# Kernel tuning notes

Hardware: AMD Instinct MI355X
Metric: run time of the kernel (lower is better)

The kernel has to match this reference:

```python
import jax, jax.numpy as jnp
import numpy as np

B, T, U = 64, 1000, 200
D, H, V = 1024, 512, 100  # decoder_dim, hidden_size, vocab_size; blank id = V
NEG = -1e30


def setup_inputs() -> dict:
    key = jax.random.key(0)
    ks = jax.random.split(key, 6)
    decoder_outputs = jax.random.normal(ks[0], (B, T, D), dtype=jnp.float32)
    target_phones = jax.random.randint(ks[1], (B, U), 0, V)
    decoder_lengths = T // 2 + jax.random.randint(ks[2], (B,), 0, T // 2 + 1)
    target_lengths = U // 2 + jax.random.randint(ks[3], (B,), 0, U // 2 + 1)
    W1 = jax.random.normal(ks[4], (H, D), dtype=jnp.float32) * (1.0 / np.sqrt(D))
    b1 = jnp.zeros((H,), jnp.float32)
    W2 = jax.random.normal(ks[5], (V + 1, H), dtype=jnp.float32) * (1.0 / np.sqrt(H))
    b2 = jnp.zeros((V + 1,), jnp.float32)
    return dict(decoder_outputs=decoder_outputs, target_phones=target_phones,
                decoder_lengths=decoder_lengths, target_lengths=target_lengths,
                W1=W1, b1=b1, W2=W2, b2=b2)


def _lse3(a, b, c):
    m = jnp.maximum(jnp.maximum(a, b), c)
    return m + jnp.log(jnp.exp(a - m) + jnp.exp(b - m) + jnp.exp(c - m))


def _ctc_loss(log_probs, targets, in_len, tgt_len, blank):
    # log_probs: [B, T, C]; targets: [B, U]; standard CTC alpha recursion in log space.
    Bb, Tt, _ = log_probs.shape
    Uu = targets.shape[1]
    S = 2 * Uu + 1  # extended label sequence: blank, y1, blank, y2, ...
    ext = jnp.full((Bb, S), blank, dtype=targets.dtype).at[:, 1::2].set(targets)
    lp = jnp.take_along_axis(log_probs, ext[:, None, :], axis=2)  # [B, T, S]
    same = jnp.concatenate([jnp.ones((Bb, 2), bool), ext[:, 2:] == ext[:, :-2]], axis=1)
    skip_ok = (ext != blank) & (~same)  # allowed s-2 transition

    a0 = jnp.full((Bb, S), NEG, jnp.float32).at[:, 0].set(lp[:, 0, 0]).at[:, 1].set(lp[:, 0, 1])
    lp_t = jnp.swapaxes(lp, 0, 1)  # [T, B, S]

    def step(alpha, xs):
        t, lpt = xs
        a1 = jnp.concatenate([jnp.full((Bb, 1), NEG, jnp.float32), alpha[:, :-1]], axis=1)
        a2 = jnp.concatenate([jnp.full((Bb, 2), NEG, jnp.float32), alpha[:, :-2]], axis=1)
        a2 = jnp.where(skip_ok, a2, NEG)
        new = _lse3(alpha, a1, a2) + lpt
        alpha = jnp.where((t < in_len)[:, None], new, alpha)  # freeze past each seq's end
        return alpha, None

    alpha, _ = jax.lax.scan(step, a0, (jnp.arange(1, Tt), lp_t[1:]))
    Sb = 2 * tgt_len + 1
    l1 = jnp.take_along_axis(alpha, (Sb - 1)[:, None], axis=1)[:, 0]
    l2 = jnp.take_along_axis(alpha, (Sb - 2)[:, None], axis=1)[:, 0]
    return -jnp.logaddexp(l1, l2)  # [B] per-sequence negative log likelihood


def reference(decoder_outputs, target_phones, decoder_lengths, target_lengths, W1, b1, W2, b2):
    # proj: Linear + ReLU (+ Dropout, identity in eval)
    h = jax.nn.relu(jnp.einsum('btd,hd->bth', decoder_outputs, W1) + b1)
    logits = jnp.einsum('bth,ch->btc', h, W2) + b2  # [B, T, V+1]
    log_probs = jax.nn.log_softmax(logits, axis=2)
    loss = _ctc_loss(log_probs, target_phones, decoder_lengths, target_lengths, blank=V)
    return jnp.mean(loss / decoder_lengths.astype(jnp.float32))
```

## Files before the change

### kernel.cpp

```cpp
#include <hip/hip_runtime.h>
#include <cstdint>
#include <cstddef>

#define NEGF (-1e30f)
#define LOG2E 1.4426950408889634f
#define LN2 0.6931471805599453f

typedef __attribute__((ext_vector_type(8))) short short8;
typedef __attribute__((ext_vector_type(4))) float f32x4;

__device__ __forceinline__ unsigned short f2bf(float f) {
  unsigned int u = __float_as_uint(f);
  u += 0x7fffu + ((u >> 16) & 1u);
  return (unsigned short)(u >> 16);
}

__device__ __forceinline__ void gload_lds16(const void* g, void* l) {
  __builtin_amdgcn_global_load_lds(
      (const __attribute__((address_space(1))) void*)g,
      (__attribute__((address_space(3))) void*)l, 16, 0, 0);
}

__device__ __forceinline__ float fexp2(float x) { return __builtin_amdgcn_exp2f(x); }
__device__ __forceinline__ float flog2(float x) { return __builtin_amdgcn_logf(x); }

__device__ __forceinline__ float wave_shr1(float x, float fill) {
  int r = __builtin_amdgcn_update_dpp(__float_as_int(fill), __float_as_int(x),
                                      0x138, 0xF, 0xF, false);
  return __int_as_float(r);
}

__device__ __forceinline__ float lse3_2(float a, float b, float c) {
  float m  = fmaxf(fmaxf(a, b), c);
  float md = __builtin_amdgcn_fmed3f(a, b, c);
  float mn = fminf(fminf(a, b), c);
  return m + flog2(fexp2(md - m) + fexp2(mn - m) + 1.0f);
}

__global__ void k_cvt(const float* __restrict__ src, unsigned short* __restrict__ dst, long n) {
  long i = ((long)blockIdx.x * blockDim.x + threadIdx.x) * 4;
  long stride = (long)gridDim.x * blockDim.x * 4;
  for (; i < n; i += stride) {
    float4 v = *(const float4*)(src + i);
    ushort4 o;
    o.x = f2bf(v.x); o.y = f2bf(v.y); o.z = f2bf(v.z); o.w = f2bf(v.w);
    *(ushort4*)(dst + i) = o;
  }
}

__global__ void k_cvt_w2(const float* __restrict__ w2, unsigned short* __restrict__ dst) {
  int i = (blockIdx.x * blockDim.x + threadIdx.x) * 4;
  if (i >= 128 * 512) return;
  int c = i >> 9;
  float4 v = make_float4(0.f, 0.f, 0.f, 0.f);
  if (c < 101) v = *(const float4*)(w2 + i);
  ushort4 o;
  o.x = f2bf(v.x); o.y = f2bf(v.y); o.z = f2bf(v.z); o.w = f2bf(v.w);
  *(ushort4*)(dst + i) = o;
}

__global__ __launch_bounds__(512, 1) void k_gemm1f(
    const float* __restrict__ X,
    const unsigned short* __restrict__ B,
    const float* __restrict__ b1,
    const int* __restrict__ dlen,
    unsigned short* __restrict__ H) {
  __shared__ __align__(16) char ldsA[128 * 144];
  __shared__ __align__(16) char ldsB[65536];
  const int K = 1024;
  int r0 = blockIdx.x * 128;
  {
    int b0 = r0 / 1000;
    int rl = r0 - b0 * 1000;
    if (rl <= 872 && rl >= dlen[b0]) return;
  }
  int tid = threadIdx.x;
  int lane = tid & 63, wid = tid >> 6;
  int wr = (wid & 1) * 64;
  int wc = (wid >> 1) * 128;

  f32x4 acc[4][8];
#pragma unroll
  for (int i = 0; i < 4; ++i)
#pragma unroll
    for (int j = 0; j < 8; ++j) acc[i][j] = (f32x4){0.f, 0.f, 0.f, 0.f};

  int arow = tid >> 2;
  int akoff = (tid & 3) * 16;

  for (int kt = 0; kt < 16; ++kt) {
    int k0 = kt * 64;
    __syncthreads();
    {
      const float* ap = X + (size_t)(r0 + arow) * K + (k0 + akoff);
      float4 av0 = *(const float4*)(ap + 0);
      float4 av1 = *(const float4*)(ap + 4);
      float4 av2 = *(const float4*)(ap + 8);
      float4 av3 = *(const float4*)(ap + 12);
      short8 as0, as1;
      as0[0] = (short)f2bf(av0.x); as0[1] = (short)f2bf(av0.y);
      as0[2] = (short)f2bf(av0.z); as0[3] = (short)f2bf(av0.w);
      as0[4] = (short)f2bf(av1.x); as0[5] = (short)f2bf(av1.y);
      as0[6] = (short)f2bf(av1.z); as0[7] = (short)f2bf(av1.w);
      as1[0] = (short)f2bf(av2.x); as1[1] = (short)f2bf(av2.y);
      as1[2] = (short)f2bf(av2.z); as1[3] = (short)f2bf(av2.w);
      as1[4] = (short)f2bf(av3.x); as1[5] = (short)f2bf(av3.y);
      as1[6] = (short)f2bf(av3.z); as1[7] = (short)f2bf(av3.w);
      int ab = arow * 144 + akoff * 2;
      *(short8*)(ldsA + ab) = as0;
      *(short8*)(ldsA + ab + 16) = as1;
    }
#pragma unroll
    for (int r = 0; r < 8; ++r) {
      int c = r * 512 + tid;
      int trow = c >> 3;
      int sch = (c & 7) ^ (trow & 7);
      gload_lds16(B + (size_t)trow * K + (k0 + sch * 8), ldsB + c * 16);
    }
    asm volatile("s_waitcnt vmcnt(0)" ::: "memory");
    __syncthreads();
#pragma unroll
    for (int kk = 0; kk < 2; ++kk) {
      int kb2 = (kk * 32 + ((lane >> 4) << 3)) * 2;
      short8 af[4], bfr[8];
#pragma unroll
      for (int i = 0; i < 4; ++i) {
        int ar = wr + i * 16 + (lane & 15);
        af[i] = *(const short8*)(ldsA + (ar * 144 + kb2));
      }
#pragma unroll
      for (int j = 0; j < 8; ++j) {
        int br = wc + j * 16 + (lane & 15);
        bfr[j] = *(const short8*)(ldsB + ((br * 128 + kb2) ^ ((br & 7) << 4)));
      }
#pragma unroll
      for (int i = 0; i < 4; ++i)
#pragma unroll
        for (int j = 0; j < 8; ++j)
          acc[i][j] = __builtin_amdgcn_mfma_f32_16x16x32_bf16(af[i], bfr[j], acc[i][j], 0, 0, 0);
    }
  }
  int cl = lane & 15, r4 = (lane >> 4) << 2;
#pragma unroll
  for (int i = 0; i < 4; ++i) {
    int row = r0 + wr + i * 16 + r4;
#pragma unroll
    for (int j = 0; j < 8; ++j) {
      int col = wc + j * 16 + cl;
      float bb = b1[col];
#pragma unroll
      for (int q = 0; q < 4; ++q) {
        float v = acc[i][j][q] + bb;
        v = v > 0.f ? v : 0.f;
        H[(size_t)(row + q) * 512 + col] = f2bf(v);
      }
    }
  }
}

__global__ __launch_bounds__(256) void k_gemm2(
    const unsigned short* __restrict__ Hm,
    const unsigned short* __restrict__ W2,
    const float* __restrict__ b2,
    const int* __restrict__ dlen,
    float* __restrict__ LPT) {
  __shared__ __align__(16) char lds[32768];
  const int K = 512;
  int row0 = blockIdx.x * 128;
  {
    int b0 = row0 / 1000;
    int rl = row0 - b0 * 1000;
    if (rl <= 872 && rl >= dlen[b0]) return;
  }
  int tid = threadIdx.x, lane = tid & 63, wid = tid >> 6;
  f32x4 acc[2][8];
#pragma unroll
  for (int i = 0; i < 2; ++i)
#pragma unroll
    for (int j = 0; j < 8; ++j) acc[i][j] = (f32x4){0.f, 0.f, 0.f, 0.f};

  for (int kt = 0; kt < 8; ++kt) {
    int k0 = kt * 64;
    __syncthreads();
#pragma unroll
    for (int r = 0; r < 4; ++r) {
      int c = r * 256 + tid;
      int trow = c >> 3;
      int sch = (c & 7) ^ (trow & 7);
      gload_lds16(Hm + (size_t)(row0 + trow) * K + (k0 + sch * 8), lds + c * 16);
      gload_lds16(W2 + (size_t)trow * K + (k0 + sch * 8), lds + 16384 + c * 16);
    }
    asm volatile("s_waitcnt vmcnt(0)" ::: "memory");
    __syncthreads();
#pragma unroll
    for (int kk = 0; kk < 2; ++kk) {
      int kb2 = (kk * 32 + ((lane >> 4) << 3)) * 2;
      short8 af[2], bfr[8];
#pragma unroll
      for (int i = 0; i < 2; ++i) {
        int ar = wid * 32 + i * 16 + (lane & 15);
        af[i] = *(const short8*)(lds + ((ar * 128 + kb2) ^ ((ar & 7) << 4)));
      }
#pragma unroll
      for (int j = 0; j < 8; ++j) {
        int br = j * 16 + (lane & 15);
        bfr[j] = *(const short8*)(lds + 16384 + ((br * 128 + kb2) ^ ((br & 7) << 4)));
      }
#pragma unroll
      for (int i = 0; i < 2; ++i)
#pragma unroll
        for (int j = 0; j < 8; ++j)
          acc[i][j] = __builtin_amdgcn_mfma_f32_16x16x32_bf16(af[i], bfr[j], acc[i][j], 0, 0, 0);
    }
  }
  int cl = lane & 15, r4 = (lane >> 4) << 2;
#pragma unroll
  for (int i = 0; i < 2; ++i) {
    float outv[4][8];
#pragma unroll
    for (int q = 0; q < 4; ++q) {
      float v[8];
      float mx = NEGF;
#pragma unroll
      for (int j = 0; j < 8; ++j) {
        int col = j * 16 + cl;
        float t = acc[i][j][q];
        if (col < 101) {
          t += b2[col];
          mx = fmaxf(mx, t);
        }
        v[j] = t;
      }
#pragma unroll
      for (int m = 1; m < 16; m <<= 1) mx = fmaxf(mx, __shfl_xor(mx, m));
      float s = 0.f;
#pragma unroll
      for (int j = 0; j < 8; ++j) {
        int col = j * 16 + cl;
        if (col < 101) s += __expf(v[j] - mx);
      }
#pragma unroll
      for (int m = 1; m < 16; m <<= 1) s += __shfl_xor(s, m);
      float lse = mx + __logf(s);
#pragma unroll
      for (int j = 0; j < 8; ++j) outv[q][j] = (v[j] - lse) * LOG2E;
    }
    int row = row0 + wid * 32 + i * 16 + r4;
    int bb = row / 1000;
    int t = row - bb * 1000;
    float* outp = LPT + (size_t)bb * 101000 + t;
#pragma unroll
    for (int j = 0; j < 8; ++j) {
      int col = j * 16 + cl;
      if (col < 101) {
        float4 o = make_float4(outv[0][j], outv[1][j], outv[2][j], outv[3][j]);
        *(float4*)(outp + col * 1000) = o;
      }
    }
  }
}

__global__ __launch_bounds__(256, 1) void k_ctc(
    const float* __restrict__ LPT,
    const int* __restrict__ tgt_all,
    const int* __restrict__ dlen,
    const int* __restrict__ tlen,
    float* __restrict__ lossout) {
  int b = blockIdx.x;
  int tid = threadIdx.x;
  int lane = tid & 63, wid = tid >> 6;
  const float* lpt = LPT + (size_t)b * 101000;
  int Tb = dlen[b];
  int Ub = tlen[b];
  const int* tg = tgt_all + b * 200;

  int h = (wid == 0) ? 0 : 16;
  int S0 = 101 * wid - h;
  int g0 = S0 + 2 * lane;

  int cls[2], sk[2];
#pragma unroll
  for (int j = 0; j < 2; ++j) {
    int s = g0 + j;
    int c = 100, skp = 0;
    if (s >= 0 && s < 401 && (s & 1)) {
      int u = (s - 1) >> 1;
      c = tg[u];
      if (s >= 3) skp = (tg[u] != tg[u - 1]) ? 1 : 0;
    }
    cls[j] = c; sk[j] = skp;
  }

  const float* pa = lpt + cls[0] * 1000;
  const float* pb = lpt + cls[1] * 1000;

  float al0 = (g0 == 0) ? pa[0] : NEGF;
  float al1 = (g0 == 0) ? pb[0] : NEGF;

  int slot_base = (wid == 0) ? 85 : 101;
  int e0 = 2 * lane - slot_base;

  __shared__ float bnd[2][3][16];
  __shared__ float sal[408];

  float4 a_lo0 = *(const float4*)(pa + 0),  a_lo1 = *(const float4*)(pa + 4);
  float4 a_hi0 = *(const float4*)(pa + 8),  a_hi1 = *(const float4*)(pa + 12);
  float4 b_lo0 = *(const float4*)(pb + 0),  b_lo1 = *(const float4*)(pb + 4);
  float4 b_hi0 = *(const float4*)(pb + 8),  b_hi1 = *(const float4*)(pb + 12);

#define STEP(tt, PA, PB)                                                  \
  do {                                                                    \
    if ((tt) < Tb) {                                                      \
      float u1 = wave_shr1(al1, NEGF);           \
      float u0 = wave_shr1(al0, NEGF);           \
      float na0 = lse3_2(al0, u1, sk[0] ? u0 : NEGF) + (PA);              \
      float na1 = lse3_2(al1, al0, sk[1] ? u1 : NEGF) + (PB);             \
      al0 = na0; al1 = na1;                                               \
    }                                                                     \
  } while (0)

  for (int t = 1; t < Tb; t += 8) {
    int buf = (t >> 3) & 1;
    if (wid < 3) {
      if (e0 >= 0 && e0 < 16) bnd[buf][wid][e0] = al0;
      int e1 = e0 + 1;
      if (e1 >= 0 && e1 < 16) bnd[buf][wid][e1] = al1;
    }
    __syncthreads();
    if (wid > 0 && lane < 8) {
      al0 = bnd[buf][wid - 1][2 * lane];
      al1 = bnd[buf][wid - 1][2 * lane + 1];
    }
    STEP(t,     a_lo0.y, b_lo0.y);
    STEP(t + 1, a_lo0.z, b_lo0.z);
    STEP(t + 2, a_lo0.w, b_lo0.w);
    STEP(t + 3, a_lo1.x, b_lo1.x);
    STEP(t + 4, a_lo1.y, b_lo1.y);
    STEP(t + 5, a_lo1.z, b_lo1.z);
    STEP(t + 6, a_lo1.w, b_lo1.w);
    STEP(t + 7, a_hi0.x, b_hi0.x);
    a_lo0 = a_hi0; a_lo1 = a_hi1;
    b_lo0 = b_hi0; b_lo1 = b_hi1;
    int tn = t + 15;
    a_hi0 = *(const float4*)(pa + tn); a_hi1 = *(const float4*)(pa + tn + 4);
    b_hi0 = *(const float4*)(pb + tn); b_hi1 = *(const float4*)(pb + tn + 4);
  }

  {
    int slot0 = 2 * lane;
    if (slot0 >= h && slot0 < h + 101 && g0 >= 0 && g0 <= 400) sal[g0] = al0;
    int slot1 = slot0 + 1, g1 = g0 + 1;
    if (slot1 >= h && slot1 < h + 101 && g1 <= 400) sal[g1] = al1;
  }
  __syncthreads();
  if (tid == 0) {
    float l1 = sal[2 * Ub];
    float l2 = sal[2 * Ub - 1];
    float m = fmaxf(l1, l2);
    float l2sum = m + flog2(fexp2(l1 - m) + fexp2(l2 - m));
    lossout[b] = (-LN2 * l2sum) / (float)Tb;
  }
#undef STEP
}

__global__ void k_reduce(const float* __restrict__ lossv, float* __restrict__ out) {
  float v = lossv[threadIdx.x];
#pragma unroll
  for (int m = 1; m < 64; m <<= 1) v += __shfl_xor(v, m);
  if (threadIdx.x == 0) out[0] = v * (1.0f / 64.0f);
}

extern "C" void kernel_launch(void* const* d_in, const int* in_sizes, int n_in,
                              void* d_out, int out_size, void* d_ws, size_t ws_size,
                              hipStream_t stream) {
  const float* X  = (const float*)d_in[0];
  const int* tgt  = (const int*)d_in[1];
  const int* dlen = (const int*)d_in[2];
  const int* tlen = (const int*)d_in[3];
  const float* W1 = (const float*)d_in[4];
  const float* b1 = (const float*)d_in[5];
  const float* W2 = (const float*)d_in[6];
  const float* b2 = (const float*)d_in[7];

  char* ws = (char*)d_ws;
  float* LPT           = (float*)(ws + 33554432);
  unsigned short* W1bf = (unsigned short*)(ws + 131072000);
  unsigned short* W2bf = (unsigned short*)(ws + 132120576);
  unsigned short* Hbf  = (unsigned short*)(ws + 132251648);
  float* lossv         = (float*)(ws + 197787648);

  k_cvt<<<512, 256, 0, stream>>>(W1, W1bf, 524288L);
  k_cvt_w2<<<64, 256, 0, stream>>>(W2, W2bf);
  k_gemm1f<<<500, 512, 0, stream>>>(X, W1bf, b1, dlen, Hbf);
  k_gemm2<<<500, 256, 0, stream>>>(Hbf, W2bf, b2, dlen, LPT);
  k_ctc<<<64, 256, 0, stream>>>(LPT, tgt, dlen, tlen, lossv);
  k_reduce<<<1, 64, 0, stream>>>(lossv, (float*)d_out);
}
```

Before: 246.2 us.

## Run CTC recursion in probability space with mantissa/exponent pairs

```diff
diff --git a/kernel.cpp b/kernel.cpp
--- a/kernel.cpp
+++ b/kernel.cpp
@@ -3,8 +3,8 @@
 #include <cstddef>
 
 #define NEGF (-1e30f)
-#define LOG2E 1.4426950408889634f
 #define LN2 0.6931471805599453f
+#define EMIN (-100000000)
 
 typedef __attribute__((ext_vector_type(8))) short short8;
 typedef __attribute__((ext_vector_type(4))) float f32x4;
@@ -29,12 +29,8 @@
                                       0x138, 0xF, 0xF, false);
   return __int_as_float(r);
 }
-
-__device__ __forceinline__ float lse3_2(float a, float b, float c) {
-  float m  = fmaxf(fmaxf(a, b), c);
-  float md = __builtin_amdgcn_fmed3f(a, b, c);
-  float mn = fminf(fminf(a, b), c);
-  return m + flog2(fexp2(md - m) + fexp2(mn - m) + 1.0f);
+__device__ __forceinline__ int wave_shr1_i(int x, int fill) {
+  return __builtin_amdgcn_update_dpp(fill, x, 0x138, 0xF, 0xF, false);
 }
 
 __global__ void k_cvt(const float* __restrict__ src, unsigned short* __restrict__ dst, long n) {
@@ -163,7 +159,7 @@
     const unsigned short* __restrict__ W2,
     const float* __restrict__ b2,
     const int* __restrict__ dlen,
-    float* __restrict__ LPT) {
+    float* __restrict__ PT) {
   __shared__ __align__(16) char lds[32768];
   const int K = 512;
   int row0 = blockIdx.x * 128;
@@ -243,12 +239,12 @@
       for (int m = 1; m < 16; m <<= 1) s += __shfl_xor(s, m);
       float lse = mx + __logf(s);
 #pragma unroll
-      for (int j = 0; j < 8; ++j) outv[q][j] = (v[j] - lse) * LOG2E;
+      for (int j = 0; j < 8; ++j) outv[q][j] = __expf(v[j] - lse);
     }
     int row = row0 + wid * 32 + i * 16 + r4;
     int bb = row / 1000;
     int t = row - bb * 1000;
-    float* outp = LPT + (size_t)bb * 101000 + t;
+    float* outp = PT + (size_t)bb * 101000 + t;
 #pragma unroll
     for (int j = 0; j < 8; ++j) {
       int col = j * 16 + cl;
@@ -261,7 +257,7 @@
 }
 
 __global__ __launch_bounds__(256, 1) void k_ctc(
-    const float* __restrict__ LPT,
+    const float* __restrict__ PT,
     const int* __restrict__ tgt_all,
     const int* __restrict__ dlen,
     const int* __restrict__ tlen,
@@ -269,7 +265,7 @@
   int b = blockIdx.x;
   int tid = threadIdx.x;
   int lane = tid & 63, wid = tid >> 6;
-  const float* lpt = LPT + (size_t)b * 101000;
+  const float* pt = PT + (size_t)b * 101000;
   int Tb = dlen[b];
   int Ub = tlen[b];
   const int* tg = tgt_all + b * 200;
@@ -291,17 +287,23 @@
     cls[j] = c; sk[j] = skp;
   }
 
-  const float* pa = lpt + cls[0] * 1000;
-  const float* pb = lpt + cls[1] * 1000;
-
-  float al0 = (g0 == 0) ? pa[0] : NEGF;
-  float al1 = (g0 == 0) ? pb[0] : NEGF;
+  const float* pa = pt + cls[0] * 1000;
+  const float* pb = pt + cls[1] * 1000;
+
+  float m0 = 0.f, m1 = 0.f;
+  int E0 = EMIN, E1 = EMIN;
+  if (g0 == 0) {
+    m0 = frexpf(pa[0], &E0);
+    m1 = frexpf(pb[0], &E1);
+  }
 
   int slot_base = (wid == 0) ? 85 : 101;
-  int e0 = 2 * lane - slot_base;
-
-  __shared__ float bnd[2][3][16];
-  __shared__ float sal[408];
+  int e0x = 2 * lane - slot_base;
+
+  __shared__ float bnd_m[2][3][16];
+  __shared__ int   bnd_e[2][3][16];
+  __shared__ float sal_m[408];
+  __shared__ int   sal_e[408];
 
   float4 a_lo0 = *(const float4*)(pa + 0),  a_lo1 = *(const float4*)(pa + 4);
   float4 a_hi0 = *(const float4*)(pa + 8),  a_hi1 = *(const float4*)(pa + 12);
@@ -311,25 +313,36 @@
 #define STEP(tt, PA, PB)                                                  \
   do {                                                                    \
     if ((tt) < Tb) {                                                      \
-      float u1 = wave_shr1(al1, NEGF);           \
-      float u0 = wave_shr1(al0, NEGF);           \
-      float na0 = lse3_2(al0, u1, sk[0] ? u0 : NEGF) + (PA);              \
-      float na1 = lse3_2(al1, al0, sk[1] ? u1 : NEGF) + (PB);             \
-      al0 = na0; al1 = na1;                                               \
+      float m1p = wave_shr1(m1, 0.f);                                     \
+      float m0p = wave_shr1(m0, 0.f);                                     \
+      int   E1p = wave_shr1_i(E1, EMIN);                                  \
+      int   E0p = wave_shr1_i(E0, EMIN);                                  \
+      float A2 = sk[0] ? m0p : 0.f;  int B2 = sk[0] ? E0p : EMIN;         \
+      int em0 = max(E0, max(E1p, B2));                                    \
+      float t0 = ldexpf(m0, E0 - em0) + ldexpf(m1p, E1p - em0)            \
+               + ldexpf(A2, B2 - em0);                                    \
+      t0 *= (PA);                                                         \
+      float C2 = sk[1] ? m1p : 0.f;  int D2 = sk[1] ? E1p : EMIN;         \
+      int em1 = max(E1, max(E0, D2));                                     \
+      float t1 = ldexpf(m1, E1 - em1) + ldexpf(m0, E0 - em1)              \
+               + ldexpf(C2, D2 - em1);                                    \
+      t1 *= (PB);                                                         \
+      int x0; m0 = frexpf(t0, &x0); E0 = em0 + x0;                        \
+      int x1; m1 = frexpf(t1, &x1); E1 = em1 + x1;                        \
     }                                                                     \
   } while (0)
 
   for (int t = 1; t < Tb; t += 8) {
     int buf = (t >> 3) & 1;
     if (wid < 3) {
-      if (e0 >= 0 && e0 < 16) bnd[buf][wid][e0] = al0;
-      int e1 = e0 + 1;
-      if (e1 >= 0 && e1 < 16) bnd[buf][wid][e1] = al1;
+      if (e0x >= 0 && e0x < 16) { bnd_m[buf][wid][e0x] = m0; bnd_e[buf][wid][e0x] = E0; }
+      int e1x = e0x + 1;
+      if (e1x >= 0 && e1x < 16) { bnd_m[buf][wid][e1x] = m1; bnd_e[buf][wid][e1x] = E1; }
     }
     __syncthreads();
     if (wid > 0 && lane < 8) {
-      al0 = bnd[buf][wid - 1][2 * lane];
-      al1 = bnd[buf][wid - 1][2 * lane + 1];
+      m0 = bnd_m[buf][wid - 1][2 * lane];     E0 = bnd_e[buf][wid - 1][2 * lane];
+      m1 = bnd_m[buf][wid - 1][2 * lane + 1]; E1 = bnd_e[buf][wid - 1][2 * lane + 1];
     }
     STEP(t,     a_lo0.y, b_lo0.y);
     STEP(t + 1, a_lo0.z, b_lo0.z);
@@ -348,17 +361,21 @@
 
   {
     int slot0 = 2 * lane;
-    if (slot0 >= h && slot0 < h + 101 && g0 >= 0 && g0 <= 400) sal[g0] = al0;
+    if (slot0 >= h && slot0 < h + 101 && g0 >= 0 && g0 <= 400) {
+      sal_m[g0] = m0; sal_e[g0] = E0;
+    }
     int slot1 = slot0 + 1, g1 = g0 + 1;
-    if (slot1 >= h && slot1 < h + 101 && g1 <= 400) sal[g1] = al1;
+    if (slot1 >= h && slot1 < h + 101 && g1 <= 400) {
+      sal_m[g1] = m1; sal_e[g1] = E1;
+    }
   }
   __syncthreads();
   if (tid == 0) {
-    float l1 = sal[2 * Ub];
-    float l2 = sal[2 * Ub - 1];
-    float m = fmaxf(l1, l2);
-    float l2sum = m + flog2(fexp2(l1 - m) + fexp2(l2 - m));
-    lossout[b] = (-LN2 * l2sum) / (float)Tb;
+    float ma = sal_m[2 * Ub], mb = sal_m[2 * Ub - 1];
+    int ea = sal_e[2 * Ub], eb = sal_e[2 * Ub - 1];
+    int em = max(ea, eb);
+    float val = ldexpf(ma, ea - em) + ldexpf(mb, eb - em);
+    lossout[b] = (-LN2 * ((float)em + flog2(val))) / (float)Tb;
   }
 #undef STEP
 }
@@ -383,7 +400,7 @@
   const float* b2 = (const float*)d_in[7];
 
   char* ws = (char*)d_ws;
-  float* LPT           = (float*)(ws + 33554432);
+  float* PT            = (float*)(ws + 33554432);
   unsigned short* W1bf = (unsigned short*)(ws + 131072000);
   unsigned short* W2bf = (unsigned short*)(ws + 132120576);
   unsigned short* Hbf  = (unsigned short*)(ws + 132251648);
@@ -392,7 +409,7 @@
   k_cvt<<<512, 256, 0, stream>>>(W1, W1bf, 524288L);
   k_cvt_w2<<<64, 256, 0, stream>>>(W2, W2bf);
   k_gemm1f<<<500, 512, 0, stream>>>(X, W1bf, b1, dlen, Hbf);
-  k_gemm2<<<500, 256, 0, stream>>>(Hbf, W2bf, b2, dlen, LPT);
-  k_ctc<<<64, 256, 0, stream>>>(LPT, tgt, dlen, tlen, lossv);
+  k_gemm2<<<500, 256, 0, stream>>>(Hbf, W2bf, b2, dlen, PT);
+  k_ctc<<<64, 256, 0, stream>>>(PT, tgt, dlen, tlen, lossv);
   k_reduce<<<1, 64, 0, stream>>>(lossv, (float*)d_out);
 }
```

Result: no change. 248.9 us (+1.1%).

## Fuse hidden projection GEMM and output GEMM with log-softmax into one kernel

Applied to the files above, without the earlier changes.

```diff
diff --git a/kernel.cpp b/kernel.cpp
--- a/kernel.cpp
+++ b/kernel.cpp
@@ -59,14 +59,17 @@
   *(ushort4*)(dst + i) = o;
 }
 
-__global__ __launch_bounds__(512, 1) void k_gemm1f(
+__global__ __launch_bounds__(512, 1) void k_fused(
     const float* __restrict__ X,
-    const unsigned short* __restrict__ B,
+    const unsigned short* __restrict__ W1b,
     const float* __restrict__ b1,
+    const unsigned short* __restrict__ W2b,
+    const float* __restrict__ b2,
     const int* __restrict__ dlen,
-    unsigned short* __restrict__ H) {
-  __shared__ __align__(16) char ldsA[128 * 144];
-  __shared__ __align__(16) char ldsB[65536];
+    float* __restrict__ LPT) {
+  __shared__ __align__(16) char lds[131072];
+  char* ldsA = lds;
+  char* ldsB = lds + 18432;
   const int K = 1024;
   int r0 = blockIdx.x * 128;
   {
@@ -115,7 +118,7 @@
       int c = r * 512 + tid;
       int trow = c >> 3;
       int sch = (c & 7) ^ (trow & 7);
-      gload_lds16(B + (size_t)trow * K + (k0 + sch * 8), ldsB + c * 16);
+      gload_lds16(W1b + (size_t)trow * K + (k0 + sch * 8), ldsB + c * 16);
     }
     asm volatile("s_waitcnt vmcnt(0)" ::: "memory");
     __syncthreads();
@@ -140,82 +143,48 @@
           acc[i][j] = __builtin_amdgcn_mfma_f32_16x16x32_bf16(af[i], bfr[j], acc[i][j], 0, 0, 0);
     }
   }
-  int cl = lane & 15, r4 = (lane >> 4) << 2;
-#pragma unroll
-  for (int i = 0; i < 4; ++i) {
-    int row = r0 + wr + i * 16 + r4;
+
+  __syncthreads();
+  {
+    int cl = lane & 15, r4 = (lane >> 4) << 2;
 #pragma unroll
     for (int j = 0; j < 8; ++j) {
-      int col = wc + j * 16 + cl;
-      float bb = b1[col];
-#pragma unroll
-      for (int q = 0; q < 4; ++q) {
-        float v = acc[i][j][q] + bb;
-        v = v > 0.f ? v : 0.f;
-        H[(size_t)(row + q) * 512 + col] = f2bf(v);
-      }
-    }
-  }
-}
-
-__global__ __launch_bounds__(256) void k_gemm2(
-    const unsigned short* __restrict__ Hm,
-    const unsigned short* __restrict__ W2,
-    const float* __restrict__ b2,
-    const int* __restrict__ dlen,
-    float* __restrict__ LPT) {
-  __shared__ __align__(16) char lds[32768];
-  const int K = 512;
-  int row0 = blockIdx.x * 128;
+      int hcol = wc + j * 16 + cl;
+      float bb = b1[hcol];
+      int cb = (hcol & 7) * 2;
+      int ch = hcol >> 3;
+#pragma unroll
+      for (int i = 0; i < 4; ++i) {
+#pragma unroll
+        for (int q = 0; q < 4; ++q) {
+          int hrow = wr + i * 16 + r4 + q;
+          float v = acc[i][j][q] + bb;
+          v = v > 0.f ? v : 0.f;
+          *(unsigned short*)(lds + hrow * 1024 + ((ch ^ (hrow & 7)) << 4) + cb) = f2bf(v);
+        }
+      }
+    }
+  }
+  __syncthreads();
+
+  f32x4 acc2[8];
+#pragma unroll
+  for (int j = 0; j < 8; ++j) acc2[j] = (f32x4){0.f, 0.f, 0.f, 0.f};
+  const char* w2c = (const char*)W2b;
+  for (int kt = 0; kt < 16; ++kt) {
+    int ar = wid * 16 + (lane & 15);
+    int ch = (kt * 4 + (lane >> 4)) ^ (ar & 7);
+    short8 af2 = *(const short8*)(lds + ar * 1024 + (ch << 4));
+#pragma unroll
+    for (int j = 0; j < 8; ++j) {
+      int bc = j * 16 + (lane & 15);
+      short8 bf2 = *(const short8*)(w2c + bc * 1024 + kt * 64 + ((lane >> 4) << 4));
+      acc2[j] = __builtin_amdgcn_mfma_f32_16x16x32_bf16(af2, bf2, acc2[j], 0, 0, 0);
+    }
+  }
+
   {
-    int b0 = row0 / 1000;
-    int rl = row0 - b0 * 1000;
-    if (rl <= 872 && rl >= dlen[b0]) return;
-  }
-  int tid = threadIdx.x, lane = tid & 63, wid = tid >> 6;
-  f32x4 acc[2][8];
-#pragma unroll
-  for (int i = 0; i < 2; ++i)
-#pragma unroll
-    for (int j = 0; j < 8; ++j) acc[i][j] = (f32x4){0.f, 0.f, 0.f, 0.f};
-
-  for (int kt = 0; kt < 8; ++kt) {
-    int k0 = kt * 64;
-    __syncthreads();
-#pragma unroll
-    for (int r = 0; r < 4; ++r) {
-      int c = r * 256 + tid;
-      int trow = c >> 3;
-      int sch = (c & 7) ^ (trow & 7);
-      gload_lds16(Hm + (size_t)(row0 + trow) * K + (k0 + sch * 8), lds + c * 16);
-      gload_lds16(W2 + (size_t)trow * K + (k0 + sch * 8), lds + 16384 + c * 16);
-    }
-    asm volatile("s_waitcnt vmcnt(0)" ::: "memory");
-    __syncthreads();
-#pragma unroll
-    for (int kk = 0; kk < 2; ++kk) {
-      int kb2 = (kk * 32 + ((lane >> 4) << 3)) * 2;
-      short8 af[2], bfr[8];
-#pragma unroll
-      for (int i = 0; i < 2; ++i) {
-        int ar = wid * 32 + i * 16 + (lane & 15);
-        af[i] = *(const short8*)(lds + ((ar * 128 + kb2) ^ ((ar & 7) << 4)));
-      }
-#pragma unroll
-      for (int j = 0; j < 8; ++j) {
-        int br = j * 16 + (lane & 15);
-        bfr[j] = *(const short8*)(lds + 16384 + ((br * 128 + kb2) ^ ((br & 7) << 4)));
-      }
-#pragma unroll
-      for (int i = 0; i < 2; ++i)
-#pragma unroll
-        for (int j = 0; j < 8; ++j)
-          acc[i][j] = __builtin_amdgcn_mfma_f32_16x16x32_bf16(af[i], bfr[j], acc[i][j], 0, 0, 0);
-    }
-  }
-  int cl = lane & 15, r4 = (lane >> 4) << 2;
-#pragma unroll
-  for (int i = 0; i < 2; ++i) {
+    int cl = lane & 15, r4 = (lane >> 4) << 2;
     float outv[4][8];
 #pragma unroll
     for (int q = 0; q < 4; ++q) {
@@ -224,7 +193,7 @@
 #pragma unroll
       for (int j = 0; j < 8; ++j) {
         int col = j * 16 + cl;
-        float t = acc[i][j][q];
+        float t = acc2[j][q];
         if (col < 101) {
           t += b2[col];
           mx = fmaxf(mx, t);
@@ -245,7 +214,7 @@
 #pragma unroll
       for (int j = 0; j < 8; ++j) outv[q][j] = (v[j] - lse) * LOG2E;
     }
-    int row = row0 + wid * 32 + i * 16 + r4;
+    int row = r0 + wid * 16 + r4;
     int bb = row / 1000;
     int t = row - bb * 1000;
     float* outp = LPT + (size_t)bb * 101000 + t;
@@ -386,13 +355,11 @@
   float* LPT           = (float*)(ws + 33554432);
   unsigned short* W1bf = (unsigned short*)(ws + 131072000);
   unsigned short* W2bf = (unsigned short*)(ws + 132120576);
-  unsigned short* Hbf  = (unsigned short*)(ws + 132251648);
   float* lossv         = (float*)(ws + 197787648);
 
   k_cvt<<<512, 256, 0, stream>>>(W1, W1bf, 524288L);
   k_cvt_w2<<<64, 256, 0, stream>>>(W2, W2bf);
-  k_gemm1f<<<500, 512, 0, stream>>>(X, W1bf, b1, dlen, Hbf);
-  k_gemm2<<<500, 256, 0, stream>>>(Hbf, W2bf, b2, dlen, LPT);
+  k_fused<<<500, 512, 0, stream>>>(X, W1bf, b1, W2bf, b2, dlen, LPT);
   k_ctc<<<64, 256, 0, stream>>>(LPT, tgt, dlen, tlen, lossv);
   k_reduce<<<1, 64, 0, stream>>>(lossv, (float*)d_out);
 }
```

Measured after the change: 265.9 us. +8.0%, slower.

## Double-buffer GEMM1 LDS tiles with register prefetch of activations

Applied to the files above, without the earlier changes.

```diff
diff --git a/kernel.cpp b/kernel.cpp
--- a/kernel.cpp
+++ b/kernel.cpp
@@ -65,8 +65,7 @@
     const float* __restrict__ b1,
     const int* __restrict__ dlen,
     unsigned short* __restrict__ H) {
-  __shared__ __align__(16) char ldsA[128 * 144];
-  __shared__ __align__(16) char ldsB[65536];
+  __shared__ __align__(16) char lds[86016];
   const int K = 1024;
   int r0 = blockIdx.x * 128;
   {
@@ -86,52 +85,66 @@
     for (int j = 0; j < 8; ++j) acc[i][j] = (f32x4){0.f, 0.f, 0.f, 0.f};
 
   int arow = tid >> 2;
-  int akoff = (tid & 3) * 16;
-
-  for (int kt = 0; kt < 16; ++kt) {
-    int k0 = kt * 64;
-    __syncthreads();
+  int akoff = (tid & 3) * 8;
+  const float* ap = X + (size_t)(r0 + arow) * K + akoff;
+  int awb = arow * 80 + (tid & 3) * 16;
+
+
+#define STAGE_A_WRITE(bufc)                                                \
+  do {                                                                     \
+    short8 as;                                                             \
+    as[0] = (short)f2bf(av0.x); as[1] = (short)f2bf(av0.y);                \
+    as[2] = (short)f2bf(av0.z); as[3] = (short)f2bf(av0.w);                \
+    as[4] = (short)f2bf(av1.x); as[5] = (short)f2bf(av1.y);                \
+    as[6] = (short)f2bf(av1.z); as[7] = (short)f2bf(av1.w);                \
+    *(short8*)(lds + (bufc) * 10240 + awb) = as;                           \
+  } while (0)
+
+#define STAGE_B(bufc, kt_)                                                 \
+  do {                                                                     \
+    _Pragma("unroll")                                                      \
+    for (int r = 0; r < 4; ++r) {                                          \
+      int c = r * 512 + tid;                                               \
+      int trow = c >> 2;                                                   \
+      int sch = (c & 3) ^ (trow & 3);                                      \
+      gload_lds16(B + (size_t)trow * K + ((kt_) * 32 + sch * 8),           \
+                  lds + 20480 + (bufc) * 32768 + c * 16);                  \
+    }                                                                      \
+  } while (0)
+
+  float4 av0 = *(const float4*)(ap + 0);
+  float4 av1 = *(const float4*)(ap + 4);
+  STAGE_A_WRITE(0);
+  STAGE_B(0, 0);
+  av0 = *(const float4*)(ap + 32);
+  av1 = *(const float4*)(ap + 36);
+  __syncthreads();
+
+  for (int kt = 0; kt < 32; ++kt) {
+    int c = kt & 1;
+    if (kt < 31) {
+      STAGE_B(c ^ 1, kt + 1);
+      STAGE_A_WRITE(c ^ 1);
+    }
+    if (kt < 30) {
+      const float* apn = ap + (kt + 2) * 32;
+      av0 = *(const float4*)(apn + 0);
+      av1 = *(const float4*)(apn + 4);
+    }
     {
-      const float* ap = X + (size_t)(r0 + arow) * K + (k0 + akoff);
-      float4 av0 = *(const float4*)(ap + 0);
-      float4 av1 = *(const float4*)(ap + 4);
-      float4 av2 = *(const float4*)(ap + 8);
-      float4 av3 = *(const float4*)(ap + 12);
-      short8 as0, as1;
-      as0[0] = (short)f2bf(av0.x); as0[1] = (short)f2bf(av0.y);
-      as0[2] = (short)f2bf(av0.z); as0[3] = (short)f2bf(av0.w);
-      as0[4] = (short)f2bf(av1.x); as0[5] = (short)f2bf(av1.y);
-      as0[6] = (short)f2bf(av1.z); as0[7] = (short)f2bf(av1.w);
-      as1[0] = (short)f2bf(av2.x); as1[1] = (short)f2bf(av2.y);
-      as1[2] = (short)f2bf(av2.z); as1[3] = (short)f2bf(av2.w);
-      as1[4] = (short)f2bf(av3.x); as1[5] = (short)f2bf(av3.y);
-      as1[6] = (short)f2bf(av3.z); as1[7] = (short)f2bf(av3.w);
-      int ab = arow * 144 + akoff * 2;
-      *(short8*)(ldsA + ab) = as0;
-      *(short8*)(ldsA + ab + 16) = as1;
-    }
-#pragma unroll
-    for (int r = 0; r < 8; ++r) {
-      int c = r * 512 + tid;
-      int trow = c >> 3;
-      int sch = (c & 7) ^ (trow & 7);
-      gload_lds16(B + (size_t)trow * K + (k0 + sch * 8), ldsB + c * 16);
-    }
-    asm volatile("s_waitcnt vmcnt(0)" ::: "memory");
-    __syncthreads();
-#pragma unroll
-    for (int kk = 0; kk < 2; ++kk) {
-      int kb2 = (kk * 32 + ((lane >> 4) << 3)) * 2;
+      const char* bufA = lds + c * 10240;
+      const char* bufB = lds + 20480 + c * 32768;
+      int kb = 16 * (lane >> 4);
       short8 af[4], bfr[8];
 #pragma unroll
       for (int i = 0; i < 4; ++i) {
         int ar = wr + i * 16 + (lane & 15);
-        af[i] = *(const short8*)(ldsA + (ar * 144 + kb2));
+        af[i] = *(const short8*)(bufA + ar * 80 + kb);
       }
 #pragma unroll
       for (int j = 0; j < 8; ++j) {
         int br = wc + j * 16 + (lane & 15);
-        bfr[j] = *(const short8*)(ldsB + ((br * 128 + kb2) ^ ((br & 7) << 4)));
+        bfr[j] = *(const short8*)(bufB + ((br * 64 + kb) ^ ((br & 3) << 4)));
       }
 #pragma unroll
       for (int i = 0; i < 4; ++i)
@@ -139,7 +152,11 @@
         for (int j = 0; j < 8; ++j)
           acc[i][j] = __builtin_amdgcn_mfma_f32_16x16x32_bf16(af[i], bfr[j], acc[i][j], 0, 0, 0);
     }
-  }
+    __syncthreads();
+  }
+#undef STAGE_A_WRITE
+#undef STAGE_B
+
   int cl = lane & 15, r4 = (lane >> 4) << 2;
 #pragma unroll
   for (int i = 0; i < 4; ++i) {
```

Result: no change. 245.2 us (-0.4%).
